# Kernel tuning notes

Measured on AMD Instinct MI355X. Metric: run time of the kernel, lower is better.

Reference implementation:

```python
import jax, jax.numpy as jnp
import numpy as np
from jax import lax

B, E, DIN = 16, 1024, 128   # batch, num_edges, link_state_dim
P, D = 2048, 128            # num_paths, path_state_dim


def _topology():
    # deterministic ragged paths: lengths in [4,16], at least one of max length 16
    lengths = 4 + (np.arange(P) % 13)
    idx = np.repeat(np.arange(P), lengths).astype(np.int32)          # path id per entry
    seqs = np.concatenate([np.arange(l) for l in lengths]).astype(np.int32)  # position in path
    paths = np.random.RandomState(0).randint(0, E, size=idx.shape[0]).astype(np.int32)
    return paths, idx, seqs


def setup_inputs() -> dict:
    key = jax.random.key(0)
    ks = jax.random.split(key, 8)
    paths, idx, seqs = _topology()
    s_in = 1.0 / np.sqrt(DIN)
    s_h = 1.0 / np.sqrt(D)
    return dict(
        inputs=jax.random.normal(ks[0], (B, E, DIN), jnp.float32),
        W_in=jax.random.normal(ks[1], (DIN, 3 * D), jnp.float32) * s_in,
        W_rec=jax.random.normal(ks[2], (D, 3 * D), jnp.float32) * s_h,
        b_in=jnp.zeros((3 * D,), jnp.float32),
        b_rec=jnp.zeros((3 * D,), jnp.float32),
        wq=jax.random.normal(ks[3], (D, D), jnp.float32) * s_h,
        wk=jax.random.normal(ks[4], (D, D), jnp.float32) * s_h,
        wv=jax.random.normal(ks[5], (D, D), jnp.float32) * s_h,
        paths=paths, idx=idx, seqs=seqs,
    )


def _forward(inputs, W_in, W_rec, b_in, b_rec, wq, wk, wv, paths, idx, seqs, max_len):
    Bc = inputs.shape[0]
    # --- ragged gather -> dense zero-padded tensor [B, P, max_len, DIN] (tf.gather + scatter_nd) ---
    h_tild = inputs[:, paths]                                  # [B, n_entries, DIN]
    link = jnp.zeros((Bc, P, max_len, DIN), inputs.dtype)
    link = link.at[:, idx, seqs].set(h_tild)
    x = link.reshape(Bc * P, max_len, DIN)                     # [BP, L, DIN]
    # --- GRU over time (keras GRUCell default: reset_after=True, tanh/sigmoid) ---
    xg = jnp.einsum('nld,de->lne', x, W_in) + b_in             # [L, BP, 3D]
    h0 = jnp.zeros((Bc * P, D), inputs.dtype)

    def step(h, xg_t):
        hg = h @ W_rec + b_rec                                 # [BP, 3D]
        xz, xr, xh = jnp.split(xg_t, 3, axis=-1)
        hz, hr, hh = jnp.split(hg, 3, axis=-1)
        z = jax.nn.sigmoid(xz + hz)
        r = jax.nn.sigmoid(xr + hr)
        hc = jnp.tanh(xh + r * hh)
        hn = z * h + (1.0 - z) * hc
        return hn, hn

    last, hs = lax.scan(step, h0, xg)                          # last:[BP,D], hs:[L,BP,D]
    hs = jnp.transpose(hs, (1, 0, 2))                          # [BP, L, D]
    # --- single-query QKV attention (raw scores, no softmax, as in source) ---
    key_ = hs @ wk                                             # [BP, L, D]
    val = hs @ wv                                              # [BP, L, D]
    q = last @ wq                                              # [BP, D]
    att = jnp.einsum('nld,nd->nl', key_, q)                    # [BP, L]
    ctx = jnp.einsum('nl,nld->nd', att, val)                   # [BP, D]
    return ctx.reshape(Bc, P, D)


def reference(inputs, W_in, W_rec, b_in, b_rec, wq, wk, wv, paths, idx, seqs):
    max_len = int(np.max(np.asarray(seqs))) + 1                # static (16)
    return _forward(inputs, W_in, W_rec, b_in, b_rec, wq, wk, wv, paths, idx, seqs, max_len)
```

## Files before the change

### kernel.cpp

```cpp
#include <hip/hip_runtime.h>
#include <hip/hip_bf16.h>
#include <cstddef>

#define P_ 2048
#define B_ 16
#define E_ 1024
#define D_ 128
#define L_ 16
#define TD_ 384

#define NEG_L2E (-1.44269504088896340736f)
#define TWO_L2E (2.88539008177792681472f)

typedef _Float16 f16x2 __attribute__((ext_vector_type(2)));
typedef _Float16 f16x8 __attribute__((ext_vector_type(8)));
typedef float    f32x4 __attribute__((ext_vector_type(4)));

__device__ __forceinline__ unsigned short f2h(float x) {
    _Float16 h = (_Float16)x;
    return __builtin_bit_cast(unsigned short, h);
}
__device__ __forceinline__ unsigned pk2(float a, float b) {
    return __builtin_bit_cast(unsigned, __builtin_amdgcn_cvt_pkrtz(a, b));
}
__device__ __forceinline__ float lo16(unsigned u) {
    return (float)__builtin_bit_cast(f16x2, u)[0];
}
__device__ __forceinline__ float hi16(unsigned u) {
    return (float)__builtin_bit_cast(f16x2, u)[1];
}
__device__ __forceinline__ float ex2(float x) {
#if __has_builtin(__builtin_amdgcn_exp2f)
    return __builtin_amdgcn_exp2f(x);
#else
    return exp2f(x);
#endif
}
__device__ __forceinline__ float dot2w(unsigned hu, unsigned qu, float c) {
#if __has_builtin(__builtin_amdgcn_fdot2)
    typedef __fp16 h2v __attribute__((ext_vector_type(2)));
    return __builtin_amdgcn_fdot2(__builtin_bit_cast(h2v, hu),
                                  __builtin_bit_cast(h2v, qu), c, false);
#else
    f16x2 h = __builtin_bit_cast(f16x2, hu), q = __builtin_bit_cast(f16x2, qu);
    return c + (float)h[0] * (float)q[0] + (float)h[1] * (float)q[1];
#endif
}

__device__ __forceinline__ void binv4(const float* __restrict__ d, float* __restrict__ o) {
    float f1 = d[0] * d[1];
    float f2 = f1 * d[2];
    float f3 = f2 * d[3];
    float r  = __builtin_amdgcn_rcpf(f3);
    o[3] = r * f2;
    float t  = r * d[3];
    o[2] = t * f1;
    float u  = t * d[2];
    o[1] = u * d[0];
    o[0] = u * d[1];
}

__device__ __forceinline__ void wf16(const float* __restrict__ src,
                                     unsigned short* __restrict__ dst, int g, int N,
                                     float sc) {
    int lane = g & 63, kt = (g >> 6) & 3, tile = g >> 8;
    int k0 = kt * 32 + (lane >> 4) * 8;
    int c = tile * 16 + (lane & 15);
#pragma unroll
    for (int j = 0; j < 8; ++j)
        dst[(size_t)g * 8 + j] = f2h(src[(size_t)(k0 + j) * N + c] * sc);
}

__device__ __forceinline__ void* hp(void* base, int t, int s, int boff) {
    return (char*)base + ((t * 16 + s) << 8) + (boff ^ ((s & 7) << 4));
}
__device__ __forceinline__ const void* hpc(const void* base, int t, int s, int boff) {
    return (const char*)base + ((t * 16 + s) << 8) + (boff ^ ((s & 7) << 4));
}

__global__ __launch_bounds__(256) void k_prep(const float* __restrict__ W_in,
                                              const float* __restrict__ wq,
                                              const float* __restrict__ wk,
                                              unsigned short* __restrict__ WfI,
                                              unsigned short* __restrict__ Mf) {
    __shared__ float wk_lds[128 * 129];
    __shared__ float wq_row2[2][128];
    int blk = blockIdx.x, tid = threadIdx.x;
    if (blk < 24) {
        int gg = blk * 256 + tid;
        wf16(W_in, WfI, gg, TD_, ((gg >> 8) < 16) ? NEG_L2E : TWO_L2E);
        return;
    }
    int j0 = (blk - 24) * 2;
    int d = tid & 127, half = tid >> 7;
    for (int r = half * 64; r < half * 64 + 64; ++r)
        wk_lds[r * 129 + d] = wk[r * 128 + d];
    wq_row2[half][d] = wq[(j0 + half) * 128 + d];
    __syncthreads();
    float acc = 0.f;
    for (int k = 0; k < 128; ++k) acc += wq_row2[half][k] * wk_lds[d * 129 + k];
    {
        int r = j0 + half;
        int tile = d >> 4, kt = r >> 5;
        int ln = ((r >> 3) & 3) * 16 + (d & 15), jj = r & 7;
        Mf[((size_t)(tile * 4 + kt) * 64 + ln) * 8 + jj] = f2h(acc);
    }
}

__global__ __launch_bounds__(256) void k_G(const float* __restrict__ inputs,
                                           const unsigned short* __restrict__ WfI,
                                           const float* __restrict__ b_in,
                                           const float* __restrict__ b_rec,
                                           unsigned short* __restrict__ G2,
                                           const float* __restrict__ W_rec,
                                           const float* __restrict__ wv,
                                           const int* __restrict__ paths,
                                           int* __restrict__ pt,
                                           unsigned short* __restrict__ WfR,
                                           unsigned short* __restrict__ wvf) {
    if (blockIdx.x >= 1024) {
        int tb = blockIdx.x - 1024, tid = threadIdx.x;
        if (tb < 128) {
            int gid = tb * 256 + tid;
            int p = gid >> 4, s = gid & 15;
            int c = p / 13, r = p - c * 13;
            int len = 4 + r;
            int off = 4 * p + 78 * c + (r * (r - 1)) / 2;
            pt[gid] = (s < len) ? paths[off + s] : E_;
        } else if (tb < 152) {
            int gg = (tb - 128) * 256 + tid;
            wf16(W_rec, WfR, gg, TD_, ((gg >> 8) < 16) ? NEG_L2E : TWO_L2E);
        } else if (tb < 160) {
            wf16(wv, wvf, (tb - 152) * 256 + tid, 128, 1.f);
        } else {
            for (int i = tid; i < 2048; i += 256) {
                int bx = i >> 7, cc = i & 127;
                size_t base = ((size_t)(bx * (E_ + 1) + E_) * 128 + cc) * 4;
                G2[base]     = f2h((b_in[cc] + b_rec[cc]) * NEG_L2E);
                G2[base + 1] = f2h((b_in[128 + cc] + b_rec[128 + cc]) * NEG_L2E);
                G2[base + 2] = f2h(b_in[256 + cc] * TWO_L2E);
                G2[base + 3] = 0;
            }
        }
        return;
    }
    __shared__ __align__(16) unsigned short a_lds[16][136];
    __shared__ __align__(16) unsigned short g_lds[16][128][4];
    int tid = threadIdx.x, w = tid >> 6, L = tid & 63;
    int l15 = L & 15, q = L >> 4;
    int row0 = blockIdx.x * 16;
    int badd = row0 >> 10;
    {
        int r = tid >> 4, c = (tid & 15) * 8;
        const float4* p = (const float4*)(inputs + (size_t)(row0 + r) * 128 + c);
        float4 v0 = p[0], v1 = p[1];
        uint4 st;
        st.x = pk2(v0.x, v0.y); st.y = pk2(v0.z, v0.w);
        st.z = pk2(v1.x, v1.y); st.w = pk2(v1.z, v1.w);
        *(uint4*)&a_lds[r][c] = st;
    }
    __syncthreads();
    f16x8 af[4];
#pragma unroll
    for (int kt = 0; kt < 4; ++kt)
        af[kt] = *(const f16x8*)&a_lds[l15][kt * 32 + q * 8];
#pragma unroll
    for (int ct = 0; ct < 6; ++ct) {
        int tl = 6 * w + ct;
        f32x4 acc = (f32x4){0.f, 0.f, 0.f, 0.f};
#pragma unroll
        for (int kt = 0; kt < 4; ++kt)
            acc = __builtin_amdgcn_mfma_f32_16x16x32_f16(
                af[kt], *(const f16x8*)(WfI + (size_t)((tl * 4 + kt) * 64 + L) * 8), acc, 0, 0, 0);
        int g  = tl >> 3;
        int dd = (tl & 7) * 16 + l15;
        float sg  = (g < 2) ? NEG_L2E : TWO_L2E;
        float bia = (b_in[tl * 16 + l15] + (g < 2 ? b_rec[tl * 16 + l15] : 0.f)) * sg;
#pragma unroll
        for (int j = 0; j < 4; ++j) {
            int r = q * 4 + j;
            g_lds[r][dd][g] = f2h(acc[j] + bia);
        }
    }
    __syncthreads();
    {
        const uint4* src = (const uint4*)g_lds;
        uint4* dst = (uint4*)(G2 + (size_t)(row0 + badd) * 512);
#pragma unroll
        for (int i = 0; i < 4; ++i) dst[tid + 256 * i] = src[tid + 256 * i];
    }
}

__global__ __launch_bounds__(512, 4) void k_rec(const unsigned short* __restrict__ WfR,
                                                const float* __restrict__ b_rec,
                                                const unsigned short* __restrict__ G2,
                                                const int* __restrict__ pt,
                                                const unsigned short* __restrict__ Mf,
                                                const unsigned short* __restrict__ wvf,
                                                float* __restrict__ out) {
    __shared__ __align__(16) unsigned short hsl[16][16][128];
    __shared__ __align__(16) unsigned short qkb[16][136];
    __shared__ __align__(16) unsigned short svb[16][136];
    __shared__ float attp[2][16][16];
    __shared__ int ofs_lds[16][16];

    int tid = threadIdx.x, w = tid >> 6, L = tid & 63;
    int l15 = L & 15, q = L >> 4;
    int c0 = 16 * w + 4 * q;
    int n0 = blockIdx.x * 16;
    int b  = n0 >> 11;
    int p0 = n0 & (P_ - 1);
    int bb = b * (E_ + 1);

    f16x8 afw[3][4];
#pragma unroll
    for (int g = 0; g < 3; ++g)
#pragma unroll
        for (int kt = 0; kt < 4; ++kt)
            afw[g][kt] = *(const f16x8*)(WfR + (size_t)(((g * 8 + w) * 4 + kt) * 64 + L) * 8);

    if (tid < 256)
        ofs_lds[tid >> 4][tid & 15] = (bb + pt[p0 * L_ + tid]) << 10;

    f32x4 rh4;
#pragma unroll
    for (int j = 0; j < 4; ++j) rh4[j] = b_rec[256 + c0 + j] * TWO_L2E;
    float h_reg[4] = {0.f, 0.f, 0.f, 0.f};
    __syncthreads();

    int ofs[16];
    {
        const uint4* op = (const uint4*)&ofs_lds[l15][0];
        uint4 o0 = op[0], o1 = op[1], o2 = op[2], o3 = op[3];
        ofs[0]  = o0.x; ofs[1]  = o0.y; ofs[2]  = o0.z; ofs[3]  = o0.w;
        ofs[4]  = o1.x; ofs[5]  = o1.y; ofs[6]  = o1.z; ofs[7]  = o1.w;
        ofs[8]  = o2.x; ofs[9]  = o2.y; ofs[10] = o2.z; ofs[11] = o2.w;
        ofs[12] = o3.x; ofs[13] = o3.y; ofs[14] = o3.z; ofs[15] = o3.w;
    }

    const char* g2c = (const char*)G2 + (size_t)c0 * 8;
    uint4 cur0 = *(const uint4*)(g2c + ofs[0]);
    uint4 cur1 = *(const uint4*)(g2c + ofs[0] + 16);

#pragma unroll
    for (int t = 0; t < L_; ++t) {
        uint4 nx0 = cur0, nx1 = cur1;
        if (t < 15) {
            const char* gp = g2c + ofs[t + 1];
            nx0 = *(const uint4*)(gp);
            nx1 = *(const uint4*)(gp + 16);
        }

        float xh[4];
        f32x4 acc[3];
        acc[0][0] = lo16(cur0.x); acc[0][1] = lo16(cur0.z);
        acc[0][2] = lo16(cur1.x); acc[0][3] = lo16(cur1.z);
        acc[1][0] = hi16(cur0.x); acc[1][1] = hi16(cur0.z);
        acc[1][2] = hi16(cur1.x); acc[1][3] = hi16(cur1.z);
        xh[0] = lo16(cur0.y); xh[1] = lo16(cur0.w);
        xh[2] = lo16(cur1.y); xh[3] = lo16(cur1.w);
        acc[2] = rh4;

        if (t > 0) {
            f16x8 hf[4];
#pragma unroll
            for (int kt = 0; kt < 4; ++kt)
                hf[kt] = *(const f16x8*)hpc(hsl, t - 1, l15, kt * 64 + q * 16);
#pragma unroll
            for (int g = 0; g < 3; ++g)
#pragma unroll
                for (int kt = 0; kt < 4; ++kt)
                    acc[g] = __builtin_amdgcn_mfma_f32_16x16x32_f16(afw[g][kt], hf[kt], acc[g], 0, 0, 0);
        }

        float dz[4], dr[4];
#pragma unroll
        for (int j = 0; j < 4; ++j) {
            dz[j] = 1.f + ex2(acc[0][j]);
            dr[j] = 1.f + ex2(acc[1][j]);
        }
        float z4[4], r4[4];
        binv4(dz, z4);
        binv4(dr, r4);
        float dh[4];
#pragma unroll
        for (int j = 0; j < 4; ++j)
            dh[j] = 1.f + ex2(fminf(xh[j] + r4[j] * acc[2][j], 30.f));
        float y4[4];
        binv4(dh, y4);
        float hn[4];
#pragma unroll
        for (int j = 0; j < 4; ++j) {
            float hc = 1.f - 2.f * y4[j];
            hn[j] = hc + z4[j] * (h_reg[j] - hc);
            h_reg[j] = hn[j];
        }
        uint2 st;
        st.x = pk2(hn[0], hn[1]); st.y = pk2(hn[2], hn[3]);
        *(uint2*)hp(hsl, t, l15, c0 * 2) = st;
        cur0 = nx0; cur1 = nx1;

        __builtin_amdgcn_wave_barrier();
        __builtin_amdgcn_s_waitcnt(0xC07F);
        __builtin_amdgcn_s_barrier();
        __builtin_amdgcn_wave_barrier();
    }

    {
        f16x8 hf[4];
#pragma unroll
        for (int kt = 0; kt < 4; ++kt)
            hf[kt] = *(const f16x8*)hpc(hsl, 15, l15, kt * 64 + q * 16);
        f32x4 a = (f32x4){0.f, 0.f, 0.f, 0.f};
#pragma unroll
        for (int kt = 0; kt < 4; ++kt)
            a = __builtin_amdgcn_mfma_f32_16x16x32_f16(
                *(const f16x8*)(Mf + (size_t)((w * 4 + kt) * 64 + L) * 8), hf[kt], a, 0, 0, 0);
        uint2 st;
        st.x = pk2(a[0], a[1]); st.y = pk2(a[2], a[3]);
        *(uint2*)&qkb[l15][c0] = st;
    }
    __syncthreads();

    {
        int s = tid & 15, l = (tid >> 4) & 15, half = tid >> 8;
        const uint4* qr = (const uint4*)&qkb[s][half * 64];
        float a = 0.f;
#pragma unroll
        for (int k8 = 0; k8 < 8; ++k8) {
            uint4 hh = *(const uint4*)hpc(hsl, l, s, half * 128 + k8 * 16);
            uint4 qq = qr[k8];
            a = dot2w(hh.x, qq.x, a); a = dot2w(hh.y, qq.y, a);
            a = dot2w(hh.z, qq.z, a); a = dot2w(hh.w, qq.w, a);
        }
        attp[half][s][l] = a;
    }
    __syncthreads();

    {
        int s = tid >> 5, d0 = (tid & 31) * 4;
        float v[4] = {0.f, 0.f, 0.f, 0.f};
#pragma unroll
        for (int l = 0; l < 16; ++l) {
            float a = attp[0][s][l] + attp[1][s][l];
            uint2 hu = *(const uint2*)hpc(hsl, l, s, d0 * 2);
            v[0] += a * lo16(hu.x); v[1] += a * hi16(hu.x);
            v[2] += a * lo16(hu.y); v[3] += a * hi16(hu.y);
        }
        uint2 st;
        st.x = pk2(v[0], v[1]); st.y = pk2(v[2], v[3]);
        *(uint2*)&svb[s][d0] = st;
    }
    __syncthreads();

    {
        f16x8 sf[4];
#pragma unroll
        for (int kt = 0; kt < 4; ++kt)
            sf[kt] = *(const f16x8*)&svb[l15][kt * 32 + q * 8];
        f32x4 a = (f32x4){0.f, 0.f, 0.f, 0.f};
#pragma unroll
        for (int kt = 0; kt < 4; ++kt)
            a = __builtin_amdgcn_mfma_f32_16x16x32_f16(
                *(const f16x8*)(wvf + (size_t)((w * 4 + kt) * 64 + L) * 8), sf[kt], a, 0, 0, 0);
        *(f32x4*)&out[(size_t)(n0 + l15) * D_ + c0] = a;
    }
}

extern "C" void kernel_launch(void* const* d_in, const int* in_sizes, int n_in,
                              void* d_out, int out_size, void* d_ws, size_t ws_size,
                              hipStream_t stream) {
    const float* inputs = (const float*)d_in[0];
    const float* W_in   = (const float*)d_in[1];
    const float* W_rec  = (const float*)d_in[2];
    const float* b_in   = (const float*)d_in[3];
    const float* b_rec  = (const float*)d_in[4];
    const float* wq     = (const float*)d_in[5];
    const float* wk     = (const float*)d_in[6];
    const float* wvp    = (const float*)d_in[7];
    const int* paths    = (const int*)d_in[8];

    const size_t off_pt  = 0;
    const size_t off_WfR = off_pt  + (size_t)P_ * L_ * 4;
    const size_t off_WfI = off_WfR + (size_t)24 * 256 * 16;
    const size_t off_Mf  = off_WfI + (size_t)24 * 256 * 16;
    const size_t off_wvf = off_Mf  + (size_t)8 * 256 * 16;
    const size_t off_G2  = off_wvf + (size_t)8 * 256 * 16;
    char* ws = (char*)d_ws;
    int* pt             = (int*)(ws + off_pt);
    unsigned short* WfR = (unsigned short*)(ws + off_WfR);
    unsigned short* WfI = (unsigned short*)(ws + off_WfI);
    unsigned short* Mf  = (unsigned short*)(ws + off_Mf);
    unsigned short* wvf = (unsigned short*)(ws + off_wvf);
    unsigned short* G2  = (unsigned short*)(ws + off_G2);
    float* out = (float*)d_out;

    k_prep<<<dim3(88), dim3(256), 0, stream>>>(W_in, wq, wk, WfI, Mf);
    k_G<<<dim3(1024 + 161), dim3(256), 0, stream>>>(inputs, WfI, b_in, b_rec, G2,
                                                    W_rec, wvp, paths, pt, WfR, wvf);
    k_rec<<<dim3(B_ * P_ / 16), dim3(512), 0, stream>>>(WfR, b_rec, G2, pt,
                                                        Mf, wvf, out);
}
```

Before: 172.7 us.

## Store input-gate table in fp32 gate-major layout and swizzle block order

The precomputed input-projection table G2 changes from fp16 interleaved [row][d][4] to fp32 gate-major [row][3][128]. This removes the fp16 unpacking in the recurrent loop and the wasted padding slot, at the cost of 1.5x more bytes per gathered row. Both kernels also remap block IDs with an XCD-style swizzle (bid&7), so neighbouring work lands on the same chip die for L2 locality. The fp32 table also gives more precise input contributions.

After: 192.9 us. 11.7% more time.

```diff
diff --git a/kernel.cpp b/kernel.cpp
--- a/kernel.cpp
+++ b/kernel.cpp
@@ -111,7 +111,7 @@
                                            const unsigned short* __restrict__ WfI,
                                            const float* __restrict__ b_in,
                                            const float* __restrict__ b_rec,
-                                           unsigned short* __restrict__ G2,
+                                           float* __restrict__ G2,
                                            const float* __restrict__ W_rec,
                                            const float* __restrict__ wv,
                                            const int* __restrict__ paths,
@@ -133,22 +133,24 @@
         } else if (tb < 160) {
             wf16(wv, wvf, (tb - 152) * 256 + tid, 128, 1.f);
         } else {
-            for (int i = tid; i < 2048; i += 256) {
-                int bx = i >> 7, cc = i & 127;
-                size_t base = ((size_t)(bx * (E_ + 1) + E_) * 128 + cc) * 4;
-                G2[base]     = f2h((b_in[cc] + b_rec[cc]) * NEG_L2E);
-                G2[base + 1] = f2h((b_in[128 + cc] + b_rec[128 + cc]) * NEG_L2E);
-                G2[base + 2] = f2h(b_in[256 + cc] * TWO_L2E);
-                G2[base + 3] = 0;
+            for (int i = tid; i < 16 * 384; i += 256) {
+                int bx = i / 384, j = i - bx * 384;
+                int g = j >> 7, cc = j & 127;
+                float v = (g == 0) ? (b_in[cc] + b_rec[cc]) * NEG_L2E
+                        : (g == 1) ? (b_in[128 + cc] + b_rec[128 + cc]) * NEG_L2E
+                                   : b_in[256 + cc] * TWO_L2E;
+                G2[(size_t)(bx * (E_ + 1) + E_) * 384 + j] = v;
             }
         }
         return;
     }
     __shared__ __align__(16) unsigned short a_lds[16][136];
-    __shared__ __align__(16) unsigned short g_lds[16][128][4];
-    int tid = threadIdx.x, w = tid >> 6, L = tid & 63;
+    __shared__ __align__(16) float g_lds[16][3][128];
+    int bid = blockIdx.x, tid = threadIdx.x;
+    int wg = ((bid & 7) << 7) | (bid >> 3);
+    int w = tid >> 6, L = tid & 63;
     int l15 = L & 15, q = L >> 4;
-    int row0 = blockIdx.x * 16;
+    int row0 = wg * 16;
     int badd = row0 >> 10;
     {
         int r = tid >> 4, c = (tid & 15) * 8;
@@ -179,21 +181,21 @@
 #pragma unroll
         for (int j = 0; j < 4; ++j) {
             int r = q * 4 + j;
-            g_lds[r][dd][g] = f2h(acc[j] + bia);
-        }
-    }
-    __syncthreads();
-    {
-        const uint4* src = (const uint4*)g_lds;
-        uint4* dst = (uint4*)(G2 + (size_t)(row0 + badd) * 512);
-#pragma unroll
-        for (int i = 0; i < 4; ++i) dst[tid + 256 * i] = src[tid + 256 * i];
+            g_lds[r][g][dd] = acc[j] + bia;
+        }
+    }
+    __syncthreads();
+    {
+        const float4* src = (const float4*)g_lds;
+        float4* dst = (float4*)G2 + (size_t)(row0 + badd) * 96;
+#pragma unroll
+        for (int i = 0; i < 6; ++i) dst[tid + 256 * i] = src[tid + 256 * i];
     }
 }
 
 __global__ __launch_bounds__(512, 4) void k_rec(const unsigned short* __restrict__ WfR,
                                                 const float* __restrict__ b_rec,
-                                                const unsigned short* __restrict__ G2,
+                                                const float* __restrict__ G2,
                                                 const int* __restrict__ pt,
                                                 const unsigned short* __restrict__ Mf,
                                                 const unsigned short* __restrict__ wvf,
@@ -207,7 +209,9 @@
     int tid = threadIdx.x, w = tid >> 6, L = tid & 63;
     int l15 = L & 15, q = L >> 4;
     int c0 = 16 * w + 4 * q;
-    int n0 = blockIdx.x * 16;
+    int bid = blockIdx.x;
+    int wg = ((bid & 7) << 8) | (bid >> 3);
+    int n0 = wg * 16;
     int b  = n0 >> 11;
     int p0 = n0 & (P_ - 1);
     int bb = b * (E_ + 1);
@@ -220,7 +224,7 @@
             afw[g][kt] = *(const f16x8*)(WfR + (size_t)(((g * 8 + w) * 4 + kt) * 64 + L) * 8);
 
     if (tid < 256)
-        ofs_lds[tid >> 4][tid & 15] = (bb + pt[p0 * L_ + tid]) << 10;
+        ofs_lds[tid >> 4][tid & 15] = (bb + pt[p0 * L_ + tid]) * 1536;
 
     f32x4 rh4;
 #pragma unroll
@@ -238,27 +242,24 @@
         ofs[12] = o3.x; ofs[13] = o3.y; ofs[14] = o3.z; ofs[15] = o3.w;
     }
 
-    const char* g2c = (const char*)G2 + (size_t)c0 * 8;
-    uint4 cur0 = *(const uint4*)(g2c + ofs[0]);
-    uint4 cur1 = *(const uint4*)(g2c + ofs[0] + 16);
+    const char* g2c = (const char*)G2 + (size_t)c0 * 4;
+    f32x4 cz = *(const f32x4*)(g2c + ofs[0]);
+    f32x4 cr = *(const f32x4*)(g2c + ofs[0] + 512);
+    f32x4 cx = *(const f32x4*)(g2c + ofs[0] + 1024);
 
 #pragma unroll
     for (int t = 0; t < L_; ++t) {
-        uint4 nx0 = cur0, nx1 = cur1;
+        f32x4 nz = cz, nr = cr, nx = cx;
         if (t < 15) {
             const char* gp = g2c + ofs[t + 1];
-            nx0 = *(const uint4*)(gp);
-            nx1 = *(const uint4*)(gp + 16);
-        }
-
-        float xh[4];
+            nz = *(const f32x4*)(gp);
+            nr = *(const f32x4*)(gp + 512);
+            nx = *(const f32x4*)(gp + 1024);
+        }
+
         f32x4 acc[3];
-        acc[0][0] = lo16(cur0.x); acc[0][1] = lo16(cur0.z);
-        acc[0][2] = lo16(cur1.x); acc[0][3] = lo16(cur1.z);
-        acc[1][0] = hi16(cur0.x); acc[1][1] = hi16(cur0.z);
-        acc[1][2] = hi16(cur1.x); acc[1][3] = hi16(cur1.z);
-        xh[0] = lo16(cur0.y); xh[1] = lo16(cur0.w);
-        xh[2] = lo16(cur1.y); xh[3] = lo16(cur1.w);
+        acc[0] = cz;
+        acc[1] = cr;
         acc[2] = rh4;
 
         if (t > 0) {
@@ -285,7 +286,7 @@
         float dh[4];
 #pragma unroll
         for (int j = 0; j < 4; ++j)
-            dh[j] = 1.f + ex2(fminf(xh[j] + r4[j] * acc[2][j], 30.f));
+            dh[j] = 1.f + ex2(fminf(cx[j] + r4[j] * acc[2][j], 30.f));
         float y4[4];
         binv4(dh, y4);
         float hn[4];
@@ -298,7 +299,7 @@
         uint2 st;
         st.x = pk2(hn[0], hn[1]); st.y = pk2(hn[2], hn[3]);
         *(uint2*)hp(hsl, t, l15, c0 * 2) = st;
-        cur0 = nx0; cur1 = nx1;
+        cz = nz; cr = nr; cx = nx;
 
         __builtin_amdgcn_wave_barrier();
         __builtin_amdgcn_s_waitcnt(0xC07F);
@@ -392,7 +393,7 @@
     unsigned short* WfI = (unsigned short*)(ws + off_WfI);
     unsigned short* Mf  = (unsigned short*)(ws + off_Mf);
     unsigned short* wvf = (unsigned short*)(ws + off_wvf);
-    unsigned short* G2  = (unsigned short*)(ws + off_G2);
+    float* G2           = (float*)(ws + off_G2);
     float* out = (float*)d_out;
 
     k_prep<<<dim3(88), dim3(256), 0, stream>>>(W_in, wq, wk, WfI, Mf);
```
